# Kernel optimization log

Hardware: AMD Instinct MI355X
Metric: run time of the kernel (lower is better)

Reference implementation:

```python
import jax, jax.numpy as jnp
import numpy as np

N_NODE = 50000
EMB = 128
LAYERS = 2
B = 1024
L = 50
E = 1_600_000


def setup_inputs() -> dict:
    key = jax.random.key(0)
    ks = jax.random.split(key, 21)
    d = EMB
    stdv = 1.0 / np.sqrt(d)
    u = lambda k, shape: jax.random.uniform(k, shape, minval=-stdv, maxval=stdv, dtype=jnp.float32)
    inp = {
        'adj_row': jax.random.randint(ks[0], (E,), 0, N_NODE, dtype=jnp.int32),
        'adj_col': jax.random.randint(ks[1], (E,), 0, N_NODE, dtype=jnp.int32),
        'adj_val': jax.random.uniform(ks[2], (E,), dtype=jnp.float32) / 32.0,  # ~row-normalized sparse adjacency
        'embedding': jax.random.normal(ks[3], (N_NODE, d), dtype=jnp.float32) * 0.1,
        'session_item': jax.random.randint(ks[4], (B, L), 0, N_NODE, dtype=jnp.int32),  # 0 hits the zero pad row
        'session_len': jnp.full((B, 1), float(L), dtype=jnp.float32),
        'D': jax.random.uniform(ks[5], (B, B), dtype=jnp.float32) / B,
        'A_sess': jax.random.uniform(ks[6], (B, B), dtype=jnp.float32) / B,
        'A_gnn': jax.random.uniform(ks[7], (B, L, 2 * L), dtype=jnp.float32) / L,
        'alias_pos': jax.random.randint(ks[8], (B, L), 0, L, dtype=jnp.int32),
        'hidden': jax.random.normal(ks[9], (B, L, d), dtype=jnp.float32) * 0.1,
        'W_in': u(ks[10], (d, d)), 'b_in': u(ks[11], (d,)),
        'W_out': u(ks[12], (d, d)), 'b_out': u(ks[13], (d,)),
        'w_ih': u(ks[14], (3 * d, 2 * d)), 'b_ih': u(ks[15], (3 * d,)),
        'w_hh': u(ks[16], (3 * d, d)), 'b_hh': u(ks[17], (3 * d,)),
        'b_iah': u(ks[18], (d,)), 'b_oah': u(ks[19], (d,)),
    }
    return inp


def reference(adj_row, adj_col, adj_val, embedding, session_item, session_len,
              D, A_sess, A_gnn, alias_pos, hidden,
              W_in, b_in, W_out, b_out, w_ih, b_ih, w_hh, b_hh, b_iah, b_oah):
    # ---- HyperConv: layers of sparse (COO) adjacency @ embedding, summed over hops ----
    emb = embedding
    final = embedding
    for _ in range(LAYERS):
        emb = jax.ops.segment_sum(adj_val[:, None] * emb[adj_col], adj_row, num_segments=N_NODE)
        final = final + emb
    item_emb = final  # [N_NODE, d]

    # ---- LineConv: zero-padded gather + mean pool over session, then session-graph propagation ----
    pad_table = jnp.concatenate([jnp.zeros((1, EMB), embedding.dtype), embedding], axis=0)
    seq_h = pad_table[session_item]                      # [B, L, d]
    sess = jnp.sum(seq_h, axis=1) / session_len          # [B, d]
    DA = D @ A_sess                                      # [B, B]
    acc = sess
    s = sess
    for _ in range(LAYERS):
        s = DA @ s
        acc = acc + s
    session_emb = acc                                    # [B, d]

    # ---- GNN: gather per-session in/out adjacency rows, gated GRU-style update ----
    in_out = jnp.take_along_axis(A_gnn, alias_pos[:, :, None], axis=1)  # [B, L, 2L]
    h_in = hidden @ W_in.T + b_in
    h_out = hidden @ W_out.T + b_out
    input_in = jnp.einsum('bij,bjd->bid', in_out[:, :, :L], h_in) + b_iah
    input_out = jnp.einsum('bij,bjd->bid', in_out[:, :, L:], h_out) + b_oah
    inputs = jnp.concatenate([input_in, input_out], axis=2)             # [B, L, 2d]
    gi = inputs @ w_ih.T + b_ih
    gh = hidden @ w_hh.T + b_hh
    i_r, i_i, i_n = jnp.split(gi, 3, axis=2)
    h_r, h_i, h_n = jnp.split(gh, 3, axis=2)
    resetgate = jax.nn.sigmoid(i_r + h_r)
    inputgate = jax.nn.sigmoid(i_i + h_i)
    newgate = jnp.tanh(i_n + resetgate * h_n)
    hy = newgate + inputgate * (hidden - newgate)        # [B, L, d]

    return item_emb, session_emb, hy
```

## Files before the change

### kernel.cpp

```cpp
#include <hip/hip_runtime.h>

#define EMB 128
#define NN 50000
#define BB 1024
#define LL 50
#define NBK 49
#define NEB 512

typedef float f32x4 __attribute__((ext_vector_type(4)));
typedef float f32x2 __attribute__((ext_vector_type(2)));
typedef unsigned short u16;
typedef unsigned int u32;
typedef unsigned long long u64;
typedef u16 u16x4 __attribute__((ext_vector_type(4)));
typedef u32 u32x4 __attribute__((ext_vector_type(4)));
typedef short bf16x8 __attribute__((ext_vector_type(8)));

__device__ __forceinline__ float u2f(u16 u) {
    union { unsigned int i; float f; } v; v.i = ((unsigned int)u) << 16; return v.f;
}
__device__ __forceinline__ u16 f2b(float f) {
    union { float f; unsigned int i; } v; v.f = f;
    unsigned int i = v.i;
    return (u16)((i + 0x7FFFu + ((i >> 16) & 1u)) >> 16);
}
__device__ __forceinline__ float lo2f(u32 w) { return u2f((u16)(w & 0xffffu)); }
__device__ __forceinline__ float hi2f(u32 w) { return u2f((u16)(w >> 16)); }
__device__ __forceinline__ float sigmoidf_(float x) { return 1.f / (1.f + __expf(-x)); }

__global__ __launch_bounds__(256) void prep_kernel(
    const float* __restrict__ emb, const float* __restrict__ A, const float* __restrict__ D,
    const float* __restrict__ whh,
    u16* __restrict__ emb_bf, u16* __restrict__ A_bf, u16* __restrict__ D_bf,
    u16* __restrict__ whh_bf,
    const int* __restrict__ rowi, int* __restrict__ bcnt,
    int E, int chunk)
{
    __shared__ int lc[NBK];
    int gid = blockIdx.x * 256 + threadIdx.x;
    int stride = gridDim.x * 256;
    int tid = threadIdx.x;
    if (blockIdx.x < NEB) {
        if (tid < NBK) lc[tid] = 0;
        __syncthreads();
        int beg = blockIdx.x * chunk, end = min(E, beg + chunk);
        for (int e = beg + tid; e < end; e += 256)
            atomicAdd(&lc[rowi[e] >> 10], 1);
        __syncthreads();
        if (tid < NBK) bcnt[blockIdx.x * NBK + tid] = lc[tid];
    }
    for (int i = gid; i < 1600000; i += stride) {
        f32x4 v = *(const f32x4*)(emb + (size_t)i * 4);
        u16x4 p;
#pragma unroll
        for (int t = 0; t < 4; t++) p[t] = f2b(v[t]);
        *(u16x4*)(emb_bf + (size_t)i * 4) = p;
    }
    for (int i = gid; i < 2146304; i += stride) {
        const float* s; u16* d; int off;
        if (i < 1048576)      { s = A;   d = A_bf;   off = i; }
        else if (i < 2097152) { s = D;   d = D_bf;   off = i - 1048576; }
        else                  { s = whh; d = whh_bf; off = i - 2097152; }
        d[off] = f2b(s[off]);
    }
}

__global__ __launch_bounds__(256) void wcomb_kernel(
    const float* __restrict__ w_ih, const float* __restrict__ W_in, const float* __restrict__ W_out,
    u16* __restrict__ WcT_bf)
{
    __shared__ float wrow[256];
    int d = blockIdx.x, c = threadIdx.x;
    wrow[c] = w_ih[d * 256 + c];
    __syncthreads();
    const float* W = (c < 128) ? W_in : W_out;
    const float* wr = wrow + ((c < 128) ? 0 : 128);
    int cc = c & 127;
    float acc = 0.f;
#pragma unroll 4
    for (int j = 0; j < 128; j++) acc += wr[j] * W[j * 128 + cc];
    WcT_bf[d * 256 + c] = f2b(acc);
}

__global__ __launch_bounds__(384) void u123_kernel(
    const float* __restrict__ w_ih, const float* __restrict__ b_in, const float* __restrict__ b_out,
    const float* __restrict__ b_iah, const float* __restrict__ b_oah, const float* __restrict__ b_ih,
    float* __restrict__ u123)
{
    int d = threadIdx.x;
    float a1 = 0.f, a2 = 0.f, a3 = 0.f;
#pragma unroll 4
    for (int j = 0; j < 128; j++) {
        float wl = w_ih[d * 256 + j], wh = w_ih[d * 256 + 128 + j];
        a1 += b_in[j] * wl;
        a2 += b_out[j] * wh;
        a3 += b_iah[j] * wl + b_oah[j] * wh;
    }
    u123[d] = a1; u123[384 + d] = a2; u123[768 + d] = a3 + b_ih[d];
}

__global__ __launch_bounds__(512) void bktscan_kernel(
    const int* __restrict__ bcnt, int* __restrict__ sofs, int* __restrict__ btot)
{
    __shared__ int ps[512];
    int k = blockIdx.x, t = threadIdx.x;
    int c = bcnt[t * NBK + k];
    ps[t] = c; __syncthreads();
    for (int off = 1; off < 512; off <<= 1) {
        int v = (t >= off) ? ps[t - off] : 0;
        __syncthreads();
        ps[t] += v; __syncthreads();
    }
    sofs[t * NBK + k] = ps[t] - c;
    if (t == 511) btot[k] = ps[511];
}

__global__ __launch_bounds__(64) void btotal_kernel(
    const int* __restrict__ btot, int* __restrict__ bofs, int E)
{
    if (threadIdx.x == 0) {
        int run = 0;
        for (int k = 0; k < NBK; k++) { bofs[k] = run; run += btot[k]; }
        bofs[NBK] = E;
    }
}

__global__ __launch_bounds__(256) void emit_kernel(
    const int* __restrict__ rowi, const int* __restrict__ coli, const float* __restrict__ val,
    const int* __restrict__ sofs, const int* __restrict__ bofs,
    u64* __restrict__ egs, int E, int chunk)
{
    __shared__ int cur[NBK];
    int b = blockIdx.x, tid = threadIdx.x;
    if (tid < NBK) cur[tid] = bofs[tid] + sofs[b * NBK + tid];
    __syncthreads();
    int beg = b * chunk, end = min(E, beg + chunk);
    for (int e = beg + tid; e < end; e += 256) {
        int r = rowi[e];
        int slot = atomicAdd(&cur[r >> 10], 1);
        u64 entry = ((u64)(u32)(r & 1023) << 32)
                  | (u64)((u32)(u16)coli[e] | ((u32)f2b(val[e]) << 16));
        egs[slot] = entry;
    }
}

__global__ __launch_bounds__(1024) void binsort2_kernel(
    const u64* __restrict__ egs, const int* __restrict__ bofs,
    int* __restrict__ row_ptr, u32* __restrict__ eg, int E)
{
    __shared__ int cnt_s[1024];
    __shared__ int ps[1024];
    int k = blockIdx.x, tid = threadIdx.x;
    int r0 = k << 10;
    int beg = bofs[k], end = bofs[k + 1];
    cnt_s[tid] = 0;
    __syncthreads();
    for (int i = beg + tid; i < end; i += 1024)
        atomicAdd(&cnt_s[(int)(egs[i] >> 32)], 1);
    __syncthreads();
    int v = cnt_s[tid];
    ps[tid] = v; __syncthreads();
    for (int off = 1; off < 1024; off <<= 1) {
        int t = (tid >= off) ? ps[tid - off] : 0;
        __syncthreads();
        ps[tid] += t; __syncthreads();
    }
    int ex = beg + ps[tid] - v;
    if (r0 + tid <= NN) row_ptr[r0 + tid] = ex;
    if (k == NBK - 1 && tid == 1023) row_ptr[NN] = E;
    cnt_s[tid] = ex;
    __syncthreads();
    for (int i = beg + tid; i < end; i += 1024) {
        u64 entry = egs[i];
        int rlo = (int)(entry >> 32);
        int p = atomicAdd(&cnt_s[rlo], 1);
        eg[p] = (u32)entry;
    }
}

template<int FUSE>
__global__ __launch_bounds__(256) void gatherb_kernel(
    const int* __restrict__ row_ptr, const u32* __restrict__ eg,
    const u16* __restrict__ src, const float* __restrict__ emb0,
    u16* __restrict__ dst_bf, float* __restrict__ dst_f)
{
    int wave = threadIdx.x >> 6;
    int lane = threadIdx.x & 63;
    int g  = lane >> 4;
    int fl = lane & 15;
    int r = blockIdx.x * 4 + wave;
    if (r >= NN) return;
    int beg = row_ptr[r], end = row_ptr[r + 1];

    float acc[8];
#pragma unroll
    for (int t = 0; t < 8; t++) acc[t] = 0.f;

    if (beg < end) {
        int last = end - 1;
        int npair = (end - beg + 7) >> 3;
        u32 pkA = eg[min(beg + g, last)];
        u32 pkB = eg[min(beg + 4 + g, last)];
        float vA = (beg + g     < end) ? u2f((u16)(pkA >> 16)) : 0.f;
        float vB = (beg + 4 + g < end) ? u2f((u16)(pkB >> 16)) : 0.f;
        u32x4 xA = *(const u32x4*)(src + ((pkA & 0xffffu) << 7) + (fl << 3));
        u32x4 xB = *(const u32x4*)(src + ((pkB & 0xffffu) << 7) + (fl << 3));
        pkA = eg[min(beg + 8  + g, last)];
        pkB = eg[min(beg + 12 + g, last)];

        int e = beg;
        for (int p = 0; p < npair; p++) {
            float cvA = vA, cvB = vB;
            u32x4 cxA = xA, cxB = xB;
            int eN = e + 8;
            vA = (eN + g     < end) ? u2f((u16)(pkA >> 16)) : 0.f;
            vB = (eN + 4 + g < end) ? u2f((u16)(pkB >> 16)) : 0.f;
            xA = *(const u32x4*)(src + ((pkA & 0xffffu) << 7) + (fl << 3));
            xB = *(const u32x4*)(src + ((pkB & 0xffffu) << 7) + (fl << 3));
            int eS = e + 16;
            pkA = eg[min(eS + g, last)];
            pkB = eg[min(eS + 4 + g, last)];
#pragma unroll
            for (int t = 0; t < 4; t++) {
                acc[2 * t]     += cvA * lo2f(cxA[t]);
                acc[2 * t + 1] += cvA * hi2f(cxA[t]);
            }
#pragma unroll
            for (int t = 0; t < 4; t++) {
                acc[2 * t]     += cvB * lo2f(cxB[t]);
                acc[2 * t + 1] += cvB * hi2f(cxB[t]);
            }
            e += 8;
        }
    }

#pragma unroll
    for (int t = 0; t < 8; t++) {
        acc[t] += __shfl_xor(acc[t], 16);
        acc[t] += __shfl_xor(acc[t], 32);
    }

    if (lane < 16) {
        if (FUSE) {
            u32x4 s = *(const u32x4*)(src + ((u32)r << 7) + (lane << 3));
            const float* e0p = emb0 + ((size_t)r << 7) + (lane << 3);
            f32x4 e0a = *(const f32x4*)e0p;
            f32x4 e0b = *(const f32x4*)(e0p + 4);
            f32x4 o0, o1;
#pragma unroll
            for (int t = 0; t < 2; t++) {
                o0[2 * t]     = acc[2 * t]     + e0a[2 * t]     + lo2f(s[t]);
                o0[2 * t + 1] = acc[2 * t + 1] + e0a[2 * t + 1] + hi2f(s[t]);
                o1[2 * t]     = acc[4 + 2 * t]     + e0b[2 * t]     + lo2f(s[2 + t]);
                o1[2 * t + 1] = acc[4 + 2 * t + 1] + e0b[2 * t + 1] + hi2f(s[2 + t]);
            }
            float* dp = dst_f + ((size_t)r << 7) + (lane << 3);
            *(f32x4*)dp = o0;
            *(f32x4*)(dp + 4) = o1;
        } else {
            u32x4 w;
#pragma unroll
            for (int t = 0; t < 4; t++)
                w[t] = (u32)f2b(acc[2 * t]) | ((u32)f2b(acc[2 * t + 1]) << 16);
            *(u32x4*)(dst_bf + ((size_t)r << 7) + (lane << 3)) = w;
        }
    }
}

__global__ __launch_bounds__(128) void sess_pool_kernel(
    const int* __restrict__ items, const float* __restrict__ emb,
    const float* __restrict__ slen, float* __restrict__ sess, u16* __restrict__ sessT)
{
    int b = blockIdx.x, d = threadIdx.x;
    const int* it = items + b * LL;
    float acc = 0.f;
    for (int l = 0; l < LL; l++) {
        int idx = it[l];
        if (idx > 0) acc += emb[(size_t)(idx - 1) * EMB + d];
    }
    float v = acc / slen[b];
    sess[b * EMB + d] = v;
    sessT[d * BB + b] = f2b(v);
}

template<int WT, int WF>
__global__ __launch_bounds__(256) void mm_mfma_kernel(
    const u16* __restrict__ M_bf, const u16* __restrict__ Xt_bf,
    u16* __restrict__ Ct_bf, float* __restrict__ C_f)
{
    int tid = threadIdx.x;
    int wv = tid >> 6, lane = tid & 63, cl = lane & 15, kg = lane >> 4;
    int rbase = blockIdx.x * 16;
    f32x4 acc[2];
    acc[0] = (f32x4)0.f; acc[1] = (f32x4)0.f;
    const u16* arow = M_bf + (size_t)(rbase + cl) * BB + kg * 8;
    const u16* brow = Xt_bf + (size_t)(wv * 32 + cl) * BB + kg * 8;
#pragma unroll 4
    for (int k0 = 0; k0 < BB; k0 += 32) {
        bf16x8 a  = *(const bf16x8*)(arow + k0);
        bf16x8 b0 = *(const bf16x8*)(brow + k0);
        bf16x8 b1 = *(const bf16x8*)(brow + (size_t)16 * BB + k0);
        acc[0] = __builtin_amdgcn_mfma_f32_16x16x32_bf16(a, b0, acc[0], 0, 0, 0);
        acc[1] = __builtin_amdgcn_mfma_f32_16x16x32_bf16(a, b1, acc[1], 0, 0, 0);
    }
#pragma unroll
    for (int nt = 0; nt < 2; nt++) {
        int col = (wv * 2 + nt) * 16 + cl;
#pragma unroll
        for (int j = 0; j < 4; j++) {
            int row = rbase + kg * 4 + j;
            if (WF) C_f[(size_t)row * EMB + col] = acc[nt][j];
            if (WT) Ct_bf[(size_t)col * BB + row] = f2b(acc[nt][j]);
        }
    }
}

__global__ __launch_bounds__(256) void out1_kernel(
    const float* __restrict__ a, const float* __restrict__ b,
    const float* __restrict__ c, float* __restrict__ o, int n)
{
    int i = blockIdx.x * 256 + threadIdx.x;
    if (i < n) o[i] = a[i] + b[i] + c[i];
}

__global__ __launch_bounds__(512) void gnn_tail_kernel(
    const float* __restrict__ hidden,
    const float* __restrict__ A_gnn, const int* __restrict__ alias_pos,
    const u16* __restrict__ WcT_bf, const u16* __restrict__ w_hh_bf,
    const float* __restrict__ u123, const float* __restrict__ b_hh,
    float* __restrict__ hy)
{
    __shared__ __attribute__((aligned(16))) u16 smem[24576];
    u16* Hs  = smem;
    u16* As  = smem + 8192;
    u16* HsT = smem + 16384;
    u16* M2s = smem + 8192;
    __shared__ float rcs[64][2];

    int b = blockIdx.x;
    int tid = threadIdx.x;
    int wv = tid >> 6, lane = tid & 63, cl = lane & 15, kg = lane >> 4;

    int pr_row[4], pr_c4[4], ppos[4];
#pragma unroll
    for (int it = 0; it < 4; it++) {
        int i = tid + it * 512;
        pr_row[it] = i >> 5; pr_c4[it] = i & 31;
        ppos[it] = (pr_row[it] < LL) ? alias_pos[b * LL + pr_row[it]] : 0;
    }
    float av[4][4];
#pragma unroll
    for (int it = 0; it < 4; it++) {
        const float* ar = A_gnn + ((size_t)b * LL + ppos[it]) * (2 * LL);
#pragma unroll
        for (int t = 0; t < 4; t++) {
            int jp = pr_c4[it] * 4 + t;
            int col = (jp < 64) ? jp : (50 + (jp - 64));
            int ok = (pr_row[it] < LL) && ((jp < 64) ? (jp < LL) : ((jp - 64) < LL));
            av[it][t] = ok ? ar[col] : 0.f;
        }
    }
    const float* hsrc = hidden + (size_t)b * LL * EMB;
    f32x4 hv[4]; int hrow[4], hc4[4];
#pragma unroll
    for (int i2 = 0; i2 < 4; i2++) {
        int lin = i2 * 512 + tid;
        hrow[i2] = lin >> 5; hc4[i2] = lin & 31;
        hv[i2] = (hrow[i2] < LL) ? *(const f32x4*)(hsrc + hrow[i2] * 128 + hc4[i2] * 4) : (f32x4)0.f;
    }
#pragma unroll
    for (int it = 0; it < 4; it++) {
        u16x4 p;
#pragma unroll
        for (int t = 0; t < 4; t++) p[t] = f2b(av[it][t]);
        *(u16x4*)((char*)As + pr_row[it] * 256 + ((pr_c4[it] * 8) ^ ((pr_row[it] & 7) << 4))) = p;
    }
#pragma unroll
    for (int i2 = 0; i2 < 4; i2++) {
        u16x4 q;
#pragma unroll
        for (int t = 0; t < 4; t++) q[t] = f2b(hv[i2][t]);
        *(u16x4*)((char*)Hs + hrow[i2] * 256 + ((hc4[i2] * 8) ^ ((hrow[i2] & 7) << 4))) = q;
#pragma unroll
        for (int t = 0; t < 4; t++) {
            int c = hc4[i2] * 4 + t;
            *(u16*)((char*)HsT + c * 128 + ((hrow[i2] * 2) ^ ((c & 7) << 4))) = q[t];
        }
    }
    __syncthreads();

    if (tid < 128) {
        int row = tid >> 1, half = tid & 1;
        float s = 0.f;
#pragma unroll
        for (int c4 = 0; c4 < 16; c4++) {
            u16x4 v = *(const u16x4*)((const char*)As + row * 256 +
                        ((half * 128 + c4 * 8) ^ ((row & 7) << 4)));
            s += u2f(v[0]) + u2f(v[1]) + u2f(v[2]) + u2f(v[3]);
        }
        rcs[row][half] = s;
    }

    {
        int h = wv >> 2, ct = wv & 3;
        f32x4 m2acc[4][2];
#pragma unroll
        for (int mt = 0; mt < 4; mt++) { m2acc[mt][0] = (f32x4)0.f; m2acc[mt][1] = (f32x4)0.f; }
#pragma unroll
        for (int ks = 0; ks < 2; ks++) {
            bf16x8 bb[2];
#pragma unroll
            for (int nt = 0; nt < 2; nt++) {
                int c = ct * 32 + nt * 16 + cl;
                bb[nt] = *(const bf16x8*)((const char*)HsT + c * 128 +
                          ((ks * 64 + kg * 16) ^ ((c & 7) << 4)));
            }
#pragma unroll
            for (int mt = 0; mt < 4; mt++) {
                int mr = mt * 16 + cl;
                bf16x8 aa = *(const bf16x8*)((const char*)As + mr * 256 +
                             ((h * 128 + ks * 64 + kg * 16) ^ ((mr & 7) << 4)));
#pragma unroll
                for (int nt = 0; nt < 2; nt++)
                    m2acc[mt][nt] = __builtin_amdgcn_mfma_f32_16x16x32_bf16(aa, bb[nt], m2acc[mt][nt], 0, 0, 0);
            }
        }
        __syncthreads();
#pragma unroll
        for (int mt = 0; mt < 4; mt++)
#pragma unroll
            for (int nt = 0; nt < 2; nt++) {
                int kcol = h * 128 + ct * 32 + nt * 16 + cl;
#pragma unroll
                for (int j = 0; j < 4; j++) {
                    int row = mt * 16 + kg * 4 + j;
                    *(u16*)((char*)M2s + row * 512 + ((kcol * 2) ^ ((row & 7) << 4))) =
                        f2b(m2acc[mt][nt][j]);
                }
            }
    }
    __syncthreads();

    f32x4 acc_ri[4][2];
    f32x4 acc_n1[4];
    f32x4 acc_n2[4];
#pragma unroll
    for (int mt = 0; mt < 4; mt++) {
        acc_ri[mt][0] = (f32x4)0.f; acc_ri[mt][1] = (f32x4)0.f;
        acc_n1[mt] = (f32x4)0.f; acc_n2[mt] = (f32x4)0.f;
    }

#pragma unroll
    for (int ks = 0; ks < 8; ks++) {
        bf16x8 a[4];
#pragma unroll
        for (int mt = 0; mt < 4; mt++) {
            int mr = mt * 16 + cl;
            a[mt] = *(const bf16x8*)((const char*)M2s + mr * 512 +
                     ((ks * 64 + kg * 16) ^ ((mr & 7) << 4)));
        }
#pragma unroll
        for (int g = 0; g < 3; g++) {
            int brow = g * 128 + wv * 16 + cl;
            bf16x8 bw = *(const bf16x8*)(WcT_bf + (size_t)brow * 256 + ks * 32 + kg * 8);
#pragma unroll
            for (int mt = 0; mt < 4; mt++) {
                f32x4* dst = (g < 2) ? &acc_ri[mt][g] : &acc_n1[mt];
                *dst = __builtin_amdgcn_mfma_f32_16x16x32_bf16(a[mt], bw, *dst, 0, 0, 0);
            }
        }
    }
#pragma unroll
    for (int ks = 0; ks < 4; ks++) {
        bf16x8 a[4];
#pragma unroll
        for (int mt = 0; mt < 4; mt++) {
            int mr = mt * 16 + cl;
            a[mt] = *(const bf16x8*)((const char*)Hs + mr * 256 +
                     ((ks * 64 + kg * 16) ^ ((mr & 7) << 4)));
        }
#pragma unroll
        for (int g = 0; g < 3; g++) {
            int brow = g * 128 + wv * 16 + cl;
            bf16x8 bw = *(const bf16x8*)(w_hh_bf + (size_t)brow * 128 + ks * 32 + kg * 8);
#pragma unroll
            for (int mt = 0; mt < 4; mt++) {
                f32x4* dst = (g < 2) ? &acc_ri[mt][g] : &acc_n2[mt];
                *dst = __builtin_amdgcn_mfma_f32_16x16x32_bf16(a[mt], bw, *dst, 0, 0, 0);
            }
        }
    }

    {
        int d = wv * 16 + cl;
        float brh = b_hh[d], bih_ = b_hh[128 + d], bnh = b_hh[256 + d];
        float u1r = u123[d],       u1i = u123[128 + d],       u1n = u123[256 + d];
        float u2r = u123[384 + d], u2i = u123[384 + 128 + d], u2n = u123[384 + 256 + d];
        float u3r = u123[768 + d], u3i = u123[768 + 128 + d], u3n = u123[768 + 256 + d];
#pragma unroll
        for (int mt = 0; mt < 4; mt++)
#pragma unroll
            for (int j = 0; j < 4; j++) {
                int row = mt * 16 + kg * 4 + j;
                if (row >= LL) continue;
                float cr = rcs[row][0], dr = rcs[row][1];
                float pr  = acc_ri[mt][0][j] + cr * u1r + dr * u2r + u3r + brh;
                float pi  = acc_ri[mt][1][j] + cr * u1i + dr * u2i + u3i + bih_;
                float pn1 = acc_n1[mt][j]    + cr * u1n + dr * u2n + u3n;
                float pn2 = acc_n2[mt][j] + bnh;
                float rg = sigmoidf_(pr);
                float ig = sigmoidf_(pi);
                float ng = tanhf(pn1 + rg * pn2);
                u16 hb = *(const u16*)((const char*)Hs + row * 256 + ((d * 2) ^ ((row & 7) << 4)));
                float h = u2f(hb);
                hy[((size_t)b * LL + row) * 128 + d] = ng + ig * (h - ng);
            }
    }
}

extern "C" void kernel_launch(void* const* d_in, const int* in_sizes, int n_in,
                              void* d_out, int out_size, void* d_ws, size_t ws_size,
                              hipStream_t stream) {
    (void)n_in; (void)out_size; (void)ws_size;
    const int*   adj_row      = (const int*)d_in[0];
    const int*   adj_col      = (const int*)d_in[1];
    const float* adj_val      = (const float*)d_in[2];
    const float* embedding    = (const float*)d_in[3];
    const int*   session_item = (const int*)d_in[4];
    const float* session_len  = (const float*)d_in[5];
    const float* Dm           = (const float*)d_in[6];
    const float* A_sess       = (const float*)d_in[7];
    const float* A_gnn        = (const float*)d_in[8];
    const int*   alias_pos    = (const int*)d_in[9];
    const float* hidden       = (const float*)d_in[10];
    const float* W_in         = (const float*)d_in[11];
    const float* b_in         = (const float*)d_in[12];
    const float* W_out        = (const float*)d_in[13];
    const float* b_out        = (const float*)d_in[14];
    const float* w_ih         = (const float*)d_in[15];
    const float* b_ih         = (const float*)d_in[16];
    const float* w_hh         = (const float*)d_in[17];
    const float* b_hh         = (const float*)d_in[18];
    const float* b_iah        = (const float*)d_in[19];
    const float* b_oah        = (const float*)d_in[20];
    const int E = in_sizes[0];

    float* out0 = (float*)d_out;
    float* out1 = out0 + 6400000;
    float* out2 = out1 + 131072;

    float* ws = (float*)d_ws;
    u16*  emb_bf  = (u16*)ws;
    int*  bcnt  = (int*)(ws + 3200000);
    int*  sofs  = (int*)(ws + 3230000);
    int*  btot  = (int*)(ws + 3260000);
    u16*  accA_bf = (u16*)(ws + 3200000);
    u32*  eg    = (u32*)(ws + 6400000);
    u64*  egs   = (u64*)(ws + 8000000);
    float* sess  = ws + 11200000;
    u16*   sessT = (u16*)(ws + 11350000);
    u16*   t1T   = (u16*)(ws + 11400000);
    u16*   s1T   = (u16*)(ws + 11450000);
    u16*   t2T   = (u16*)(ws + 11500000);
    float* s1    = ws + 11550000;
    float* s2    = ws + 11700000;
    u16*   A_bf  = (u16*)(ws + 11850000);
    u16*   D_bf  = (u16*)(ws + 12400000);
    int*   row_ptr = (int*)(ws + 12950000);
    int*   bofs    = row_ptr + NN + 1;
    u16* WcT_bf    = (u16*)(ws + 13107200);
    u16* w_hh_bf   = WcT_bf + 98304;
    float* u123    = (float*)(w_hh_bf + 49152);

    int chunk = (E + NEB - 1) / NEB;

    prep_kernel<<<2048, 256, 0, stream>>>(embedding, A_sess, Dm, w_hh,
                                          emb_bf, A_bf, D_bf, w_hh_bf,
                                          adj_row, bcnt, E, chunk);
    wcomb_kernel<<<384, 256, 0, stream>>>(w_ih, W_in, W_out, WcT_bf);
    u123_kernel<<<1, 384, 0, stream>>>(w_ih, b_in, b_out, b_iah, b_oah, b_ih, u123);

    bktscan_kernel<<<NBK, 512, 0, stream>>>(bcnt, sofs, btot);
    btotal_kernel<<<1, 64, 0, stream>>>(btot, bofs, E);
    emit_kernel<<<NEB, 256, 0, stream>>>(adj_row, adj_col, adj_val, sofs, bofs, egs, E, chunk);
    binsort2_kernel<<<NBK, 1024, 0, stream>>>(egs, bofs, row_ptr, eg, E);
    gatherb_kernel<0><<<(NN + 3) / 4, 256, 0, stream>>>(row_ptr, eg, emb_bf, embedding, accA_bf, (float*)nullptr);
    gatherb_kernel<1><<<(NN + 3) / 4, 256, 0, stream>>>(row_ptr, eg, accA_bf, embedding, (u16*)nullptr, out0);

    sess_pool_kernel<<<BB, 128, 0, stream>>>(session_item, embedding, session_len, sess, sessT);
    mm_mfma_kernel<1, 0><<<64, 256, 0, stream>>>(A_bf, sessT, t1T, (float*)nullptr);
    mm_mfma_kernel<1, 1><<<64, 256, 0, stream>>>(D_bf, t1T, s1T, s1);
    mm_mfma_kernel<1, 0><<<64, 256, 0, stream>>>(A_bf, s1T, t2T, (float*)nullptr);
    mm_mfma_kernel<0, 1><<<64, 256, 0, stream>>>(D_bf, t2T, (u16*)nullptr, s2);
    out1_kernel<<<(131072 + 255) / 256, 256, 0, stream>>>(sess, s1, s2, out1, 131072);

    gnn_tail_kernel<<<BB, 512, 0, stream>>>(hidden, A_gnn, alias_pos,
                                            WcT_bf, w_hh_bf, u123, b_hh, out2);
}
```

Baseline: 340.0 us.

## Fold weight-combine and bias kernels into prep; pad transposed hidden tile; fast tanh

Merges the wcomb and u123 precompute kernels into extra blocks of the prep kernel, removing two launches and their serialization on the stream. The GNN tail now builds the transposed hidden tile in shared memory by reading hidden directly from global memory in column order and writing packed 4-element chunks into a padded layout (stride 72), replacing scalar swizzled stores. It also replaces tanhf with an exp-based tanh. The transposed loads from global are strided and may be less coalesced, and the exp-based tanh can overflow to NaN for large negative inputs.

```diff
diff --git a/kernel.cpp b/kernel.cpp
--- a/kernel.cpp
+++ b/kernel.cpp
@@ -6,6 +6,7 @@
 #define LL 50
 #define NBK 49
 #define NEB 512
+#define NCONV 2048
 
 typedef float f32x4 __attribute__((ext_vector_type(4)));
 typedef float f32x2 __attribute__((ext_vector_type(2)));
@@ -27,6 +28,10 @@
 __device__ __forceinline__ float lo2f(u32 w) { return u2f((u16)(w & 0xffffu)); }
 __device__ __forceinline__ float hi2f(u32 w) { return u2f((u16)(w >> 16)); }
 __device__ __forceinline__ float sigmoidf_(float x) { return 1.f / (1.f + __expf(-x)); }
+__device__ __forceinline__ float tanhf_(float x) {
+    float e = __expf(-2.f * x);
+    return (1.f - e) / (1.f + e);
+}
 
 __global__ __launch_bounds__(256) void prep_kernel(
     const float* __restrict__ emb, const float* __restrict__ A, const float* __restrict__ D,
@@ -34,12 +39,52 @@
     u16* __restrict__ emb_bf, u16* __restrict__ A_bf, u16* __restrict__ D_bf,
     u16* __restrict__ whh_bf,
     const int* __restrict__ rowi, int* __restrict__ bcnt,
+    const float* __restrict__ w_ih, const float* __restrict__ W_in, const float* __restrict__ W_out,
+    const float* __restrict__ b_in, const float* __restrict__ b_out,
+    const float* __restrict__ b_iah, const float* __restrict__ b_oah, const float* __restrict__ b_ih,
+    u16* __restrict__ WcT_bf, float* __restrict__ u123,
     int E, int chunk)
 {
     __shared__ int lc[NBK];
-    int gid = blockIdx.x * 256 + threadIdx.x;
-    int stride = gridDim.x * 256;
+    __shared__ float wrow[256];
+    __shared__ float red[3][256];
     int tid = threadIdx.x;
+
+    if (blockIdx.x >= NCONV) {
+        int d = blockIdx.x - NCONV;
+        int c = tid;
+        wrow[c] = w_ih[d * 256 + c];
+        __syncthreads();
+        const float* W = (c < 128) ? W_in : W_out;
+        const float* wr = wrow + ((c < 128) ? 0 : 128);
+        int cc = c & 127;
+        float acc = 0.f;
+#pragma unroll 4
+        for (int j = 0; j < 128; j++) acc += wr[j] * W[j * 128 + cc];
+        WcT_bf[d * 256 + c] = f2b(acc);
+        float p1 = (c < 128) ? b_in[c] * wrow[c] : 0.f;
+        float p2 = (c >= 128) ? b_out[cc] * wrow[c] : 0.f;
+        float p3 = (c < 128) ? b_iah[c] * wrow[c] : b_oah[cc] * wrow[c];
+        red[0][c] = p1; red[1][c] = p2; red[2][c] = p3;
+        __syncthreads();
+        for (int off = 128; off > 0; off >>= 1) {
+            if (c < off) {
+                red[0][c] += red[0][c + off];
+                red[1][c] += red[1][c + off];
+                red[2][c] += red[2][c + off];
+            }
+            __syncthreads();
+        }
+        if (c == 0) {
+            u123[d] = red[0][0];
+            u123[384 + d] = red[1][0];
+            u123[768 + d] = red[2][0] + b_ih[d];
+        }
+        return;
+    }
+
+    int gid = blockIdx.x * 256 + tid;
+    int stride = NCONV * 256;
     if (blockIdx.x < NEB) {
         if (tid < NBK) lc[tid] = 0;
         __syncthreads();
@@ -63,40 +108,6 @@
         else                  { s = whh; d = whh_bf; off = i - 2097152; }
         d[off] = f2b(s[off]);
     }
-}
-
-__global__ __launch_bounds__(256) void wcomb_kernel(
-    const float* __restrict__ w_ih, const float* __restrict__ W_in, const float* __restrict__ W_out,
-    u16* __restrict__ WcT_bf)
-{
-    __shared__ float wrow[256];
-    int d = blockIdx.x, c = threadIdx.x;
-    wrow[c] = w_ih[d * 256 + c];
-    __syncthreads();
-    const float* W = (c < 128) ? W_in : W_out;
-    const float* wr = wrow + ((c < 128) ? 0 : 128);
-    int cc = c & 127;
-    float acc = 0.f;
-#pragma unroll 4
-    for (int j = 0; j < 128; j++) acc += wr[j] * W[j * 128 + cc];
-    WcT_bf[d * 256 + c] = f2b(acc);
-}
-
-__global__ __launch_bounds__(384) void u123_kernel(
-    const float* __restrict__ w_ih, const float* __restrict__ b_in, const float* __restrict__ b_out,
-    const float* __restrict__ b_iah, const float* __restrict__ b_oah, const float* __restrict__ b_ih,
-    float* __restrict__ u123)
-{
-    int d = threadIdx.x;
-    float a1 = 0.f, a2 = 0.f, a3 = 0.f;
-#pragma unroll 4
-    for (int j = 0; j < 128; j++) {
-        float wl = w_ih[d * 256 + j], wh = w_ih[d * 256 + 128 + j];
-        a1 += b_in[j] * wl;
-        a2 += b_out[j] * wh;
-        a3 += b_iah[j] * wl + b_oah[j] * wh;
-    }
-    u123[d] = a1; u123[384 + d] = a2; u123[768 + d] = a3 + b_ih[d];
 }
 
 __global__ __launch_bounds__(512) void bktscan_kernel(
@@ -330,7 +341,7 @@
     const float* __restrict__ u123, const float* __restrict__ b_hh,
     float* __restrict__ hy)
 {
-    __shared__ __attribute__((aligned(16))) u16 smem[24576];
+    __shared__ __attribute__((aligned(16))) u16 smem[25600];
     u16* Hs  = smem;
     u16* As  = smem + 8192;
     u16* HsT = smem + 16384;
@@ -381,11 +392,19 @@
 #pragma unroll
         for (int t = 0; t < 4; t++) q[t] = f2b(hv[i2][t]);
         *(u16x4*)((char*)Hs + hrow[i2] * 256 + ((hc4[i2] * 8) ^ ((hrow[i2] & 7) << 4))) = q;
-#pragma unroll
-        for (int t = 0; t < 4; t++) {
-            int c = hc4[i2] * 4 + t;
-            *(u16*)((char*)HsT + c * 128 + ((hrow[i2] * 2) ^ ((c & 7) << 4))) = q[t];
-        }
+    }
+#pragma unroll
+    for (int i2 = 0; i2 < 4; i2++) {
+        int idx = i2 * 512 + tid;
+        int c = idx & 127, rg = idx >> 7;
+        int r0 = rg * 4;
+        u16x4 p = (u16x4)0;
+#pragma unroll
+        for (int k = 0; k < 4; k++) {
+            int row = r0 + k;
+            p[k] = (row < LL) ? f2b(hsrc[row * 128 + c]) : (u16)0;
+        }
+        *(u16x4*)&HsT[c * 72 + r0] = p;
     }
     __syncthreads();
 
@@ -412,8 +431,7 @@
 #pragma unroll
             for (int nt = 0; nt < 2; nt++) {
                 int c = ct * 32 + nt * 16 + cl;
-                bb[nt] = *(const bf16x8*)((const char*)HsT + c * 128 +
-                          ((ks * 64 + kg * 16) ^ ((c & 7) << 4)));
+                bb[nt] = *(const bf16x8*)&HsT[c * 72 + ks * 32 + kg * 8];
             }
 #pragma unroll
             for (int mt = 0; mt < 4; mt++) {
@@ -510,7 +528,7 @@
                 float pn2 = acc_n2[mt][j] + bnh;
                 float rg = sigmoidf_(pr);
                 float ig = sigmoidf_(pi);
-                float ng = tanhf(pn1 + rg * pn2);
+                float ng = tanhf_(pn1 + rg * pn2);
                 u16 hb = *(const u16*)((const char*)Hs + row * 256 + ((d * 2) ^ ((row & 7) << 4)));
                 float h = u2f(hb);
                 hy[((size_t)b * LL + row) * 128 + d] = ng + ig * (h - ng);
@@ -574,11 +592,12 @@
 
     int chunk = (E + NEB - 1) / NEB;
 
-    prep_kernel<<<2048, 256, 0, stream>>>(embedding, A_sess, Dm, w_hh,
+    prep_kernel<<<NCONV + 384, 256, 0, stream>>>(embedding, A_sess, Dm, w_hh,
                                           emb_bf, A_bf, D_bf, w_hh_bf,
-                                          adj_row, bcnt, E, chunk);
-    wcomb_kernel<<<384, 256, 0, stream>>>(w_ih, W_in, W_out, WcT_bf);
-    u123_kernel<<<1, 384, 0, stream>>>(w_ih, b_in, b_out, b_iah, b_oah, b_ih, u123);
+                                          adj_row, bcnt,
+                                          w_ih, W_in, W_out, b_in, b_out, b_iah, b_oah, b_ih,
+                                          WcT_bf, u123,
+                                          E, chunk);
 
     bktscan_kernel<<<NBK, 512, 0, stream>>>(bcnt, sofs, btot);
     btotal_kernel<<<1, 64, 0, stream>>>(btot, bofs, E);
```

After: 314.8 us. 7.4% less time.
